# Kernel tuning notes

Measured on AMD Instinct MI355X. Metric: run time of the kernel, lower is better.

## Reference

```python
import jax, jax.numpy as jnp
from jax import lax
import numpy as np

T, B, I, H, O = 512, 128, 256, 512, 256


def setup_inputs() -> dict:
    key = jax.random.key(0)
    ks = jax.random.split(key, 11)
    s = 0.05
    return {
        "x": jax.random.normal(ks[0], (T, B, I), dtype=jnp.float32),
        "W_ih0": jax.random.normal(ks[1], (H, I), dtype=jnp.float32) * s,
        "b_ih0": jax.random.normal(ks[2], (H,), dtype=jnp.float32) * s,
        "W_hh0": jax.random.normal(ks[3], (H, H), dtype=jnp.float32) * s,
        "b_hh0": jax.random.normal(ks[4], (H,), dtype=jnp.float32) * s,
        "W_ih1": jax.random.normal(ks[5], (H, H), dtype=jnp.float32) * s,
        "b_ih1": jax.random.normal(ks[6], (H,), dtype=jnp.float32) * s,
        "W_hh1": jax.random.normal(ks[7], (H, H), dtype=jnp.float32) * s,
        "b_hh1": jax.random.normal(ks[8], (H,), dtype=jnp.float32) * s,
        "W_fc": jax.random.normal(ks[9], (O, H), dtype=jnp.float32) * s,
        "b_fc": jax.random.normal(ks[10], (O,), dtype=jnp.float32) * s,
    }


def reference(x, W_ih0, b_ih0, W_hh0, b_hh0, W_ih1, b_ih1, W_hh1, b_hh1, W_fc, b_fc):
    # x: [T, B, I] (batch_first=False). 2-layer tanh RNN via lax.scan over time.
    Tn, Bn, _ = x.shape
    Hn = W_hh0.shape[0]
    h0 = jnp.zeros((2, Bn, Hn), dtype=x.dtype)

    def step(h, xt):
        h1 = jnp.tanh(xt @ W_ih0.T + b_ih0 + h[0] @ W_hh0.T + b_hh0)  # [B, H]
        h2 = jnp.tanh(h1 @ W_ih1.T + b_ih1 + h[1] @ W_hh1.T + b_hh1)  # [B, H]
        return jnp.stack([h1, h2]), h2

    h_final, out = lax.scan(step, h0, x)  # out: [T, B, H]
    # Faithful to source: output[:, -1, :] indexes the LAST BATCH element (batch_first=False),
    # giving [T, H]; pred is [T, O].
    pred = out[:, -1, :] @ W_fc.T + b_fc
    return pred, h_final
```

## Files before the change

### kernel.cpp

```cpp
#include <hip/hip_runtime.h>
#include <hip/hip_bf16.h>

#define TT 512
#define BB 128
#define II 256
#define HH 512
#define OO 256

#define NGB 8
#define NGN 16
#define NS  32

#define PRED_SZ (TT*OO)

typedef __attribute__((ext_vector_type(8))) short bf16x8;
typedef __attribute__((ext_vector_type(4))) float f32x4;
typedef __attribute__((ext_vector_type(4))) int   i32x4;
typedef __attribute__((ext_vector_type(2))) int   i32x2;

#define WS_F1   0
#define WS_F2   1024
#define WS_H1   2048
#define WS_H2   (WS_H1 + 4*BB*HH*2)
#define WS_SAVE (WS_H2 + 2*BB*HH*2)
#define WS_ZERO WS_SAVE

__device__ __forceinline__ ushort f2bf(float f) {
  union { float f; unsigned u; } v; v.f = f;
  unsigned u = v.u;
  return (ushort)((u + 0x7FFFu + ((u >> 16) & 1u)) >> 16);
}

__device__ __forceinline__ float fast_tanh(float x) {
  float cx = fminf(fmaxf(x, -30.f), 30.f);
  float t  = __builtin_amdgcn_exp2f(cx * 2.885390081777927f);
  return (t - 1.f) * __builtin_amdgcn_rcpf(t + 1.f);
}

__device__ __forceinline__ i32x4 ld16(const ushort* p) {
  i32x4 r;
  asm volatile("global_load_dwordx4 %0, %1, off sc0 sc1" : "=v"(r) : "v"(p) : "memory");
  return r;
}
__device__ __forceinline__ f32x4 ld16g(const float* p) {
  f32x4 r;
  asm volatile("global_load_dwordx4 %0, %1, off" : "=v"(r) : "v"(p));
  return r;
}
__device__ __forceinline__ void st8(ushort* p, i32x2 v) {
  asm volatile("global_store_dwordx2 %0, %1, off sc0 sc1" :: "v"(p), "v"(v) : "memory");
}
__device__ __forceinline__ void st_flag(int* p, int v) {
  asm volatile("global_store_dword %0, %1, off sc0 sc1" :: "v"(p), "v"(v) : "memory");
}
__device__ __forceinline__ int ld_flag(const int* p) {
  int r;
  asm volatile("global_load_dword %0, %1, off sc0 sc1\n\ts_waitcnt vmcnt(0)"
               : "=v"(r) : "v"(p) : "memory");
  return r;
}
#define WAIT_VM(N) asm volatile("s_waitcnt vmcnt(" #N ")" ::: "memory")

__global__ __launch_bounds__(256, 1) void rnn_scan_kernel(
    const float* __restrict__ x,
    const float* __restrict__ Wih0, const float* __restrict__ bih0,
    const float* __restrict__ Whh0, const float* __restrict__ bhh0,
    const float* __restrict__ Wih1, const float* __restrict__ bih1,
    const float* __restrict__ Whh1, const float* __restrict__ bhh1,
    float* __restrict__ out, char* __restrict__ ws)
{
  __shared__ ushort ldsW[112*64*8];
  __shared__ float bias0[NS];
  __shared__ float bias1[NS];

  int*    flag1  = (int*)(ws + WS_F1);
  int*    flag2  = (int*)(ws + WS_F2);
  ushort* h1buf  = (ushort*)(ws + WS_H1);
  ushort* h2buf  = (ushort*)(ws + WS_H2);
  float*  h2save = (float*)(ws + WS_SAVE);

  const int tid  = threadIdx.x;
  const int bid  = blockIdx.x;
  const int gb   = bid & 7;
  const int gn   = bid >> 3;
  const int n0   = gn * NS;
  const int lane = tid & 63;

  {
    const int q = tid >> 6;
    #pragma unroll 1
    for (int u = 0; u < 112; ++u) {
      const float* Wsrc; int Km; int ul;
      if (u < 16)      { Wsrc = Wih0; Km = II; ul = u; }
      else if (u < 48) { Wsrc = Whh0; Km = HH; ul = u - 16; }
      else if (u < 80) { Wsrc = Wih1; Km = HH; ul = u - 48; }
      else             { Wsrc = Whh1; Km = HH; ul = u - 80; }
      const int nk  = Km >> 5;
      const int ttl = ul / nk;
      const int kk  = ul - ttl*nk;
      const int n   = n0 + ttl*16 + (lane & 15);
      const int k   = kk*32 + (lane >> 4)*8 + q*2;
      const float2 wv = *(const float2*)(Wsrc + (size_t)n*Km + k);
      ushort2 b2; b2.x = f2bf(wv.x); b2.y = f2bf(wv.y);
      *(ushort2*)&ldsW[(u*64 + lane)*8 + q*2] = b2;
    }
    if (tid < NS) {
      bias0[tid] = bih0[n0+tid] + bhh0[n0+tid];
      bias1[tid] = bih1[n0+tid] + bhh1[n0+tid];
    }
  }
  __syncthreads();

  const int w     = tid >> 6;
  const int ttile = w & 1;
  const int layer = w >> 1;
  const int kq    = lane >> 4;
  const int c     = lane & 15;
  const int rowg  = gb*16 + c;
  const int fl32  = lane & 31;
  const int nn    = ttile*16 + kq*4;
  int* f1g = flag1 + gb*32;
  int* f2g = flag2 + gb*32;
  const int myf = gn*2 + ttile;

  if (layer == 0) {
    f32x4 xacc = {0.f,0.f,0.f,0.f};
    {
      const float* xp = x + (size_t)rowg*II + kq*8;
      f32x4 xv[16];
      #pragma unroll
      for (int kk = 0; kk < 8; ++kk) {
        xv[2*kk]   = ld16g(xp + kk*32);
        xv[2*kk+1] = ld16g(xp + kk*32 + 4);
      }
      WAIT_VM(0);
      __builtin_amdgcn_sched_barrier(0);
      #pragma unroll
      for (int kk = 0; kk < 8; ++kk) {
        bf16x8 a;
        #pragma unroll
        for (int j = 0; j < 4; ++j) {
          a[j]   = (short)f2bf(xv[2*kk][j]);
          a[j+4] = (short)f2bf(xv[2*kk+1][j]);
        }
        const bf16x8 wf = *(const bf16x8*)&ldsW[((ttile*8 + kk)*64 + lane)*8];
        xacc = __builtin_amdgcn_mfma_f32_16x16x32_bf16(wf, a, xacc, 0, 0, 0);
      }
    }

    int vf1 = 0, vf2 = 0;
    for (int p = 0; p < TT; ++p) {
      if (p >= 1 && !__all(vf1 >= p)) {
        do { vf1 = ld_flag(f1g + fl32); } while (!__all(vf1 >= p));
      }
      if (p >= 4 && !__all(vf2 >= p-3)) {
        do { __builtin_amdgcn_s_sleep(1); vf2 = ld_flag(f2g + fl32); } while (!__all(vf2 >= p-3));
      }
      i32x4 af[16];
      if (p >= 1) {
        const ushort* ap = h1buf + ((size_t)((p-1)&3)*BB + rowg)*HH + kq*8;
        #pragma unroll
        for (int kk = 0; kk < 16; ++kk) af[kk] = ld16(ap + kk*32);
      }
      const int pn = (p+1 < TT) ? (p+1) : (TT-1);
      f32x4 xv[16];
      {
        const float* xp = x + ((size_t)pn*BB + rowg)*II + kq*8;
        #pragma unroll
        for (int kk = 0; kk < 8; ++kk) {
          xv[2*kk]   = ld16g(xp + kk*32);
          xv[2*kk+1] = ld16g(xp + kk*32 + 4);
        }
      }
      f32x4 ac1 = {0.f,0.f,0.f,0.f}, ac2 = {0.f,0.f,0.f,0.f};
      if (p >= 1) {
        WAIT_VM(16);
        __builtin_amdgcn_sched_barrier(0);
        #pragma unroll
        for (int kk = 0; kk < 8; ++kk) {
          const bf16x8 b0 = *(const bf16x8*)&ldsW[((16 + ttile*16 + kk)*64 + lane)*8];
          const bf16x8 b1 = *(const bf16x8*)&ldsW[((16 + ttile*16 + kk + 8)*64 + lane)*8];
          ac1 = __builtin_amdgcn_mfma_f32_16x16x32_bf16(b0, __builtin_bit_cast(bf16x8, af[kk]),   ac1, 0, 0, 0);
          ac2 = __builtin_amdgcn_mfma_f32_16x16x32_bf16(b1, __builtin_bit_cast(bf16x8, af[kk+8]), ac2, 0, 0, 0);
        }
      }
      float v0 = fast_tanh(xacc[0] + ac1[0] + ac2[0] + bias0[nn+0]);
      float v1 = fast_tanh(xacc[1] + ac1[1] + ac2[1] + bias0[nn+1]);
      float v2 = fast_tanh(xacc[2] + ac1[2] + ac2[2] + bias0[nn+2]);
      float v3 = fast_tanh(xacc[3] + ac1[3] + ac2[3] + bias0[nn+3]);
      i32x2 d;
      d[0] = (int)((unsigned)f2bf(v0) | ((unsigned)f2bf(v1) << 16));
      d[1] = (int)((unsigned)f2bf(v2) | ((unsigned)f2bf(v3) << 16));
      st8(h1buf + (size_t)(p&3)*BB*HH + (size_t)rowg*HH + n0 + nn, d);
      if (p == TT-1) {
        *(f32x4*)&out[PRED_SZ + (size_t)rowg*HH + n0 + nn] = (f32x4){v0,v1,v2,v3};
      }
      WAIT_VM(1);
      __builtin_amdgcn_sched_barrier(0);
      f32x4 xn = {0.f,0.f,0.f,0.f};
      #pragma unroll
      for (int kk = 0; kk < 8; ++kk) {
        bf16x8 a;
        #pragma unroll
        for (int j = 0; j < 4; ++j) {
          a[j]   = (short)f2bf(xv[2*kk][j]);
          a[j+4] = (short)f2bf(xv[2*kk+1][j]);
        }
        const bf16x8 wf = *(const bf16x8*)&ldsW[((ttile*8 + kk)*64 + lane)*8];
        xn = __builtin_amdgcn_mfma_f32_16x16x32_bf16(wf, a, xn, 0, 0, 0);
      }
      WAIT_VM(0);
      if (lane == 0) st_flag(&f1g[myf], p + 1);
      xacc = xn;
    }
  } else {
    int vf1 = 0, vf2 = 0;
    for (int p = 1; p <= TT; ++p) {
      if (!__all(vf1 >= p)) {
        do { vf1 = ld_flag(f1g + fl32); } while (!__all(vf1 >= p));
      }
      if (p >= 2 && !__all(vf2 >= p-1)) {
        do { vf2 = ld_flag(f2g + fl32); } while (!__all(vf2 >= p-1));
      }
      i32x4 af[16], a2[16];
      const ushort* ap  = h1buf + ((size_t)((p-1)&3)*BB + rowg)*HH + kq*8;
      const ushort* a2p = h2buf + ((size_t)(p&1)*BB + rowg)*HH + kq*8;
      #pragma unroll
      for (int kk = 0; kk < 16; ++kk) {
        af[kk] = ld16(ap  + kk*32);
        a2[kk] = ld16(a2p + kk*32);
      }
      WAIT_VM(0);
      __builtin_amdgcn_sched_barrier(0);

      f32x4 ac1 = {0.f,0.f,0.f,0.f}, ac2 = {0.f,0.f,0.f,0.f};
      f32x4 ac3 = {0.f,0.f,0.f,0.f}, ac4 = {0.f,0.f,0.f,0.f};
      #pragma unroll
      for (int kk = 0; kk < 8; ++kk) {
        const bf16x8 b0 = *(const bf16x8*)&ldsW[((48 + ttile*16 + kk)*64 + lane)*8];
        const bf16x8 b1 = *(const bf16x8*)&ldsW[((48 + ttile*16 + kk + 8)*64 + lane)*8];
        const bf16x8 b2 = *(const bf16x8*)&ldsW[((80 + ttile*16 + kk)*64 + lane)*8];
        const bf16x8 b3 = *(const bf16x8*)&ldsW[((80 + ttile*16 + kk + 8)*64 + lane)*8];
        ac1 = __builtin_amdgcn_mfma_f32_16x16x32_bf16(b0, __builtin_bit_cast(bf16x8, af[kk]),   ac1, 0, 0, 0);
        ac2 = __builtin_amdgcn_mfma_f32_16x16x32_bf16(b1, __builtin_bit_cast(bf16x8, af[kk+8]), ac2, 0, 0, 0);
        ac3 = __builtin_amdgcn_mfma_f32_16x16x32_bf16(b2, __builtin_bit_cast(bf16x8, a2[kk]),   ac3, 0, 0, 0);
        ac4 = __builtin_amdgcn_mfma_f32_16x16x32_bf16(b3, __builtin_bit_cast(bf16x8, a2[kk+8]), ac4, 0, 0, 0);
      }
      float v0 = fast_tanh(ac1[0] + ac2[0] + ac3[0] + ac4[0] + bias1[nn+0]);
      float v1 = fast_tanh(ac1[1] + ac2[1] + ac3[1] + ac4[1] + bias1[nn+1]);
      float v2 = fast_tanh(ac1[2] + ac2[2] + ac3[2] + ac4[2] + bias1[nn+2]);
      float v3 = fast_tanh(ac1[3] + ac2[3] + ac3[3] + ac4[3] + bias1[nn+3]);
      i32x2 d;
      d[0] = (int)((unsigned)f2bf(v0) | ((unsigned)f2bf(v1) << 16));
      d[1] = (int)((unsigned)f2bf(v2) | ((unsigned)f2bf(v3) << 16));
      st8(h2buf + (size_t)((p-1)&1)*BB*HH + (size_t)rowg*HH + n0 + nn, d);
      if (rowg == BB-1) {
        *(f32x4*)&h2save[(size_t)(p-1)*HH + n0 + nn] = (f32x4){v0,v1,v2,v3};
      }
      if (p == TT) {
        *(f32x4*)&out[PRED_SZ + BB*HH + (size_t)rowg*HH + n0 + nn] = (f32x4){v0,v1,v2,v3};
      }
      WAIT_VM(0);
      if (lane == 0) st_flag(&f2g[myf], p);
    }
  }
}

__global__ __launch_bounds__(256) void rnn_pred_kernel(
    const float* __restrict__ Wfc, const float* __restrict__ bfc,
    const float* __restrict__ h2save, float* __restrict__ out)
{
  __shared__ float hs[HH];
  const int t = blockIdx.x;
  for (int i = threadIdx.x; i < HH; i += 256) hs[i] = h2save[(size_t)t*HH + i];
  __syncthreads();
  const int o = threadIdx.x;
  const f32x4* wr = (const f32x4*)(Wfc + (size_t)o*HH);
  f32x4 s = {0.f,0.f,0.f,0.f};
  #pragma unroll 8
  for (int k = 0; k < HH/4; ++k) {
    const f32x4 wv = wr[k];
    const f32x4 hv = *(const f32x4*)&hs[4*k];
    s += wv * hv;
  }
  out[(size_t)t*OO + o] = bfc[o] + s[0] + s[1] + s[2] + s[3];
}

extern "C" void kernel_launch(void* const* d_in, const int* in_sizes, int n_in,
                              void* d_out, int out_size, void* d_ws, size_t ws_size,
                              hipStream_t stream) {
  const float* x    = (const float*)d_in[0];
  const float* Wih0 = (const float*)d_in[1];
  const float* bih0 = (const float*)d_in[2];
  const float* Whh0 = (const float*)d_in[3];
  const float* bhh0 = (const float*)d_in[4];
  const float* Wih1 = (const float*)d_in[5];
  const float* bih1 = (const float*)d_in[6];
  const float* Whh1 = (const float*)d_in[7];
  const float* bhh1 = (const float*)d_in[8];
  const float* Wfc  = (const float*)d_in[9];
  const float* bfc  = (const float*)d_in[10];
  float* out = (float*)d_out;
  char*  ws  = (char*)d_ws;

  hipMemsetAsync(ws, 0, WS_ZERO, stream);

  rnn_scan_kernel<<<NGB*NGN, 256, 0, stream>>>(x, Wih0, bih0, Whh0, bhh0,
                                               Wih1, bih1, Whh1, bhh1, out, ws);
  rnn_pred_kernel<<<TT, 256, 0, stream>>>(Wfc, bfc, (const float*)(ws + WS_SAVE), out);
}
```

Measured before the change: 3.912 ms.

## Replace per-step flag handshakes with tagged hidden-state words for inline validity

Each hidden-state element is stored as a 32-bit word holding the bf16 value in the high half and an 8-bit step tag in the low half. Consumers poll the data itself until every tag matches, which drops the separate layer-0 flag and the store-wait-flag round trip on the critical path. Layer-1 now signals consumption of h1 early, before its matmul, and the h2 ring buffer grows to four slots. In exchange the h1/h2 traffic doubles in size and byte-permute unpacking is added before each MFMA.

Result: slower. 5.513 ms (+40.9%).

```diff
diff --git a/kernel.cpp b/kernel.cpp
--- a/kernel.cpp
+++ b/kernel.cpp
@@ -16,14 +16,13 @@
 typedef __attribute__((ext_vector_type(8))) short bf16x8;
 typedef __attribute__((ext_vector_type(4))) float f32x4;
 typedef __attribute__((ext_vector_type(4))) int   i32x4;
-typedef __attribute__((ext_vector_type(2))) int   i32x2;
-
-#define WS_F1   0
-#define WS_F2   1024
+
+#define WS_F2   0
 #define WS_H1   2048
-#define WS_H2   (WS_H1 + 4*BB*HH*2)
-#define WS_SAVE (WS_H2 + 2*BB*HH*2)
+#define WS_H2   (WS_H1 + 4*BB*HH*4)
+#define WS_SAVE (WS_H2 + 4*BB*HH*4)
 #define WS_ZERO WS_SAVE
+
 
 __device__ __forceinline__ ushort f2bf(float f) {
   union { float f; unsigned u; } v; v.f = f;
@@ -37,7 +36,7 @@
   return (t - 1.f) * __builtin_amdgcn_rcpf(t + 1.f);
 }
 
-__device__ __forceinline__ i32x4 ld16(const ushort* p) {
+__device__ __forceinline__ i32x4 ld16f(const int* p) {
   i32x4 r;
   asm volatile("global_load_dwordx4 %0, %1, off sc0 sc1" : "=v"(r) : "v"(p) : "memory");
   return r;
@@ -47,8 +46,8 @@
   asm volatile("global_load_dwordx4 %0, %1, off" : "=v"(r) : "v"(p));
   return r;
 }
-__device__ __forceinline__ void st8(ushort* p, i32x2 v) {
-  asm volatile("global_store_dwordx2 %0, %1, off sc0 sc1" :: "v"(p), "v"(v) : "memory");
+__device__ __forceinline__ void st16(int* p, i32x4 v) {
+  asm volatile("global_store_dwordx4 %0, %1, off sc0 sc1" :: "v"(p), "v"(v) : "memory");
 }
 __device__ __forceinline__ void st_flag(int* p, int v) {
   asm volatile("global_store_dword %0, %1, off sc0 sc1" :: "v"(p), "v"(v) : "memory");
@@ -60,6 +59,16 @@
   return r;
 }
 #define WAIT_VM(N) asm volatile("s_waitcnt vmcnt(" #N ")" ::: "memory")
+
+__device__ __forceinline__ bf16x8 fragw(const i32x4* a, int q) {
+  const i32x4 lo = a[2*q], hi = a[2*q+1];
+  i32x4 r;
+  r[0] = (int)__builtin_amdgcn_perm((unsigned)lo[1], (unsigned)lo[0], 0x07060302u);
+  r[1] = (int)__builtin_amdgcn_perm((unsigned)lo[3], (unsigned)lo[2], 0x07060302u);
+  r[2] = (int)__builtin_amdgcn_perm((unsigned)hi[1], (unsigned)hi[0], 0x07060302u);
+  r[3] = (int)__builtin_amdgcn_perm((unsigned)hi[3], (unsigned)hi[2], 0x07060302u);
+  return __builtin_bit_cast(bf16x8, r);
+}
 
 __global__ __launch_bounds__(256, 1) void rnn_scan_kernel(
     const float* __restrict__ x,
@@ -73,11 +82,10 @@
   __shared__ float bias0[NS];
   __shared__ float bias1[NS];
 
-  int*    flag1  = (int*)(ws + WS_F1);
-  int*    flag2  = (int*)(ws + WS_F2);
-  ushort* h1buf  = (ushort*)(ws + WS_H1);
-  ushort* h2buf  = (ushort*)(ws + WS_H2);
-  float*  h2save = (float*)(ws + WS_SAVE);
+  int*   flag2  = (int*)(ws + WS_F2);
+  int*   h1f    = (int*)(ws + WS_H1);
+  int*   h2f    = (int*)(ws + WS_H2);
+  float* h2save = (float*)(ws + WS_SAVE);
 
   const int tid  = threadIdx.x;
   const int bid  = blockIdx.x;
@@ -119,7 +127,6 @@
   const int rowg  = gb*16 + c;
   const int fl32  = lane & 31;
   const int nn    = ttile*16 + kq*4;
-  int* f1g = flag1 + gb*32;
   int* f2g = flag2 + gb*32;
   const int myf = gn*2 + ttile;
 
@@ -148,19 +155,52 @@
       }
     }
 
-    int vf1 = 0, vf2 = 0;
+    int vf2 = 0;
     for (int p = 0; p < TT; ++p) {
-      if (p >= 1 && !__all(vf1 >= p)) {
-        do { vf1 = ld_flag(f1g + fl32); } while (!__all(vf1 >= p));
-      }
+      i32x4 af[32];
+      if (p >= 1) {
+        const int* ap = h1f + ((size_t)((p-1)&3)*BB + rowg)*HH + kq*8;
+        const int expl = p & 255;
+        const int* f2p = f2g + fl32;
+        for (;;) {
+          #pragma unroll
+          for (int kk = 0; kk < 16; ++kk) {
+            af[2*kk]   = ld16f(ap + kk*32);
+            af[2*kk+1] = ld16f(ap + kk*32 + 4);
+          }
+          int f2v = vf2;
+          if (p >= 4) {
+            asm volatile("global_load_dword %0, %1, off sc0 sc1" : "=v"(f2v) : "v"(f2p) : "memory");
+          }
+          WAIT_VM(0);
+          __builtin_amdgcn_sched_barrier(0);
+          int bad = 0;
+          #pragma unroll
+          for (int q = 0; q < 32; ++q)
+            bad |= (af[q][0]^expl) | (af[q][1]^expl) | (af[q][2]^expl) | (af[q][3]^expl);
+          vf2 = f2v;
+          if (__all((bad & 255) == 0)) break;
+          __builtin_amdgcn_s_sleep(1);
+        }
+      }
+      f32x4 ac1 = {0.f,0.f,0.f,0.f}, ac2 = {0.f,0.f,0.f,0.f};
+      if (p >= 1) {
+        #pragma unroll
+        for (int kk = 0; kk < 8; ++kk) {
+          const bf16x8 a0 = fragw(af, kk);
+          const bf16x8 a1 = fragw(af, kk+8);
+          const bf16x8 b0 = *(const bf16x8*)&ldsW[((16 + ttile*16 + kk)*64 + lane)*8];
+          const bf16x8 b1 = *(const bf16x8*)&ldsW[((16 + ttile*16 + kk + 8)*64 + lane)*8];
+          ac1 = __builtin_amdgcn_mfma_f32_16x16x32_bf16(b0, a0, ac1, 0, 0, 0);
+          ac2 = __builtin_amdgcn_mfma_f32_16x16x32_bf16(b1, a1, ac2, 0, 0, 0);
+        }
+      }
+      const float v0 = fast_tanh(xacc[0] + ac1[0] + ac2[0] + bias0[nn+0]);
+      const float v1 = fast_tanh(xacc[1] + ac1[1] + ac2[1] + bias0[nn+1]);
+      const float v2 = fast_tanh(xacc[2] + ac1[2] + ac2[2] + bias0[nn+2]);
+      const float v3 = fast_tanh(xacc[3] + ac1[3] + ac2[3] + bias0[nn+3]);
       if (p >= 4 && !__all(vf2 >= p-3)) {
-        do { __builtin_amdgcn_s_sleep(1); vf2 = ld_flag(f2g + fl32); } while (!__all(vf2 >= p-3));
-      }
-      i32x4 af[16];
-      if (p >= 1) {
-        const ushort* ap = h1buf + ((size_t)((p-1)&3)*BB + rowg)*HH + kq*8;
-        #pragma unroll
-        for (int kk = 0; kk < 16; ++kk) af[kk] = ld16(ap + kk*32);
+        do { vf2 = ld_flag(f2g + fl32); } while (!__all(vf2 >= p-3));
       }
       const int pn = (p+1 < TT) ? (p+1) : (TT-1);
       f32x4 xv[16];
@@ -172,29 +212,13 @@
           xv[2*kk+1] = ld16g(xp + kk*32 + 4);
         }
       }
-      f32x4 ac1 = {0.f,0.f,0.f,0.f}, ac2 = {0.f,0.f,0.f,0.f};
-      if (p >= 1) {
-        WAIT_VM(16);
-        __builtin_amdgcn_sched_barrier(0);
-        #pragma unroll
-        for (int kk = 0; kk < 8; ++kk) {
-          const bf16x8 b0 = *(const bf16x8*)&ldsW[((16 + ttile*16 + kk)*64 + lane)*8];
-          const bf16x8 b1 = *(const bf16x8*)&ldsW[((16 + ttile*16 + kk + 8)*64 + lane)*8];
-          ac1 = __builtin_amdgcn_mfma_f32_16x16x32_bf16(b0, __builtin_bit_cast(bf16x8, af[kk]),   ac1, 0, 0, 0);
-          ac2 = __builtin_amdgcn_mfma_f32_16x16x32_bf16(b1, __builtin_bit_cast(bf16x8, af[kk+8]), ac2, 0, 0, 0);
-        }
-      }
-      float v0 = fast_tanh(xacc[0] + ac1[0] + ac2[0] + bias0[nn+0]);
-      float v1 = fast_tanh(xacc[1] + ac1[1] + ac2[1] + bias0[nn+1]);
-      float v2 = fast_tanh(xacc[2] + ac1[2] + ac2[2] + bias0[nn+2]);
-      float v3 = fast_tanh(xacc[3] + ac1[3] + ac2[3] + bias0[nn+3]);
-      i32x2 d;
-      d[0] = (int)((unsigned)f2bf(v0) | ((unsigned)f2bf(v1) << 16));
-      d[1] = (int)((unsigned)f2bf(v2) | ((unsigned)f2bf(v3) << 16));
-      st8(h1buf + (size_t)(p&3)*BB*HH + (size_t)rowg*HH + n0 + nn, d);
-      if (p == TT-1) {
-        *(f32x4*)&out[PRED_SZ + (size_t)rowg*HH + n0 + nn] = (f32x4){v0,v1,v2,v3};
-      }
+      const int tg = (p+1) & 255;
+      i32x4 d;
+      d[0] = ((int)(unsigned)f2bf(v0) << 16) | tg;
+      d[1] = ((int)(unsigned)f2bf(v1) << 16) | tg;
+      d[2] = ((int)(unsigned)f2bf(v2) << 16) | tg;
+      d[3] = ((int)(unsigned)f2bf(v3) << 16) | tg;
+      st16(h1f + (size_t)(p&3)*BB*HH + (size_t)rowg*HH + n0 + nn, d);
       WAIT_VM(1);
       __builtin_amdgcn_sched_barrier(0);
       f32x4 xn = {0.f,0.f,0.f,0.f};
@@ -209,59 +233,90 @@
         const bf16x8 wf = *(const bf16x8*)&ldsW[((ttile*8 + kk)*64 + lane)*8];
         xn = __builtin_amdgcn_mfma_f32_16x16x32_bf16(wf, a, xn, 0, 0, 0);
       }
-      WAIT_VM(0);
-      if (lane == 0) st_flag(&f1g[myf], p + 1);
       xacc = xn;
+      if (p == TT-1) {
+        *(f32x4*)&out[PRED_SZ + (size_t)rowg*HH + n0 + nn] = (f32x4){v0,v1,v2,v3};
+      }
     }
   } else {
-    int vf1 = 0, vf2 = 0;
     for (int p = 1; p <= TT; ++p) {
-      if (!__all(vf1 >= p)) {
-        do { vf1 = ld_flag(f1g + fl32); } while (!__all(vf1 >= p));
-      }
-      if (p >= 2 && !__all(vf2 >= p-1)) {
-        do { vf2 = ld_flag(f2g + fl32); } while (!__all(vf2 >= p-1));
-      }
-      i32x4 af[16], a2[16];
-      const ushort* ap  = h1buf + ((size_t)((p-1)&3)*BB + rowg)*HH + kq*8;
-      const ushort* a2p = h2buf + ((size_t)(p&1)*BB + rowg)*HH + kq*8;
-      #pragma unroll
-      for (int kk = 0; kk < 16; ++kk) {
-        af[kk] = ld16(ap  + kk*32);
-        a2[kk] = ld16(a2p + kk*32);
-      }
-      WAIT_VM(0);
-      __builtin_amdgcn_sched_barrier(0);
+      bf16x8 fa2[16];
+      {
+        i32x4 a2[32];
+        const int* a2p = h2f + ((size_t)((p+2)&3)*BB + rowg)*HH + kq*8;
+        const int expl = (p-1) & 255;
+        for (;;) {
+          #pragma unroll
+          for (int kk = 0; kk < 16; ++kk) {
+            a2[2*kk]   = ld16f(a2p + kk*32);
+            a2[2*kk+1] = ld16f(a2p + kk*32 + 4);
+          }
+          WAIT_VM(0);
+          __builtin_amdgcn_sched_barrier(0);
+          int bad = 0;
+          #pragma unroll
+          for (int q = 0; q < 32; ++q)
+            bad |= (a2[q][0]^expl) | (a2[q][1]^expl) | (a2[q][2]^expl) | (a2[q][3]^expl);
+          if (__all((bad & 255) == 0)) break;
+          __builtin_amdgcn_s_sleep(1);
+        }
+        #pragma unroll
+        for (int kk = 0; kk < 16; ++kk) fa2[kk] = fragw(a2, kk);
+      }
+      i32x4 af[32];
+      {
+        const int* ap = h1f + ((size_t)((p-1)&3)*BB + rowg)*HH + kq*8;
+        const int expl = p & 255;
+        for (;;) {
+          #pragma unroll
+          for (int kk = 0; kk < 16; ++kk) {
+            af[2*kk]   = ld16f(ap + kk*32);
+            af[2*kk+1] = ld16f(ap + kk*32 + 4);
+          }
+          WAIT_VM(0);
+          __builtin_amdgcn_sched_barrier(0);
+          int bad = 0;
+          #pragma unroll
+          for (int q = 0; q < 32; ++q)
+            bad |= (af[q][0]^expl) | (af[q][1]^expl) | (af[q][2]^expl) | (af[q][3]^expl);
+          if (__all((bad & 255) == 0)) break;
+          __builtin_amdgcn_s_sleep(1);
+        }
+      }
+      if (lane == 0) st_flag(&f2g[myf], p);
 
       f32x4 ac1 = {0.f,0.f,0.f,0.f}, ac2 = {0.f,0.f,0.f,0.f};
       f32x4 ac3 = {0.f,0.f,0.f,0.f}, ac4 = {0.f,0.f,0.f,0.f};
       #pragma unroll
       for (int kk = 0; kk < 8; ++kk) {
+        const bf16x8 a0 = fragw(af, kk);
+        const bf16x8 a1 = fragw(af, kk+8);
         const bf16x8 b0 = *(const bf16x8*)&ldsW[((48 + ttile*16 + kk)*64 + lane)*8];
         const bf16x8 b1 = *(const bf16x8*)&ldsW[((48 + ttile*16 + kk + 8)*64 + lane)*8];
         const bf16x8 b2 = *(const bf16x8*)&ldsW[((80 + ttile*16 + kk)*64 + lane)*8];
         const bf16x8 b3 = *(const bf16x8*)&ldsW[((80 + ttile*16 + kk + 8)*64 + lane)*8];
-        ac1 = __builtin_amdgcn_mfma_f32_16x16x32_bf16(b0, __builtin_bit_cast(bf16x8, af[kk]),   ac1, 0, 0, 0);
-        ac2 = __builtin_amdgcn_mfma_f32_16x16x32_bf16(b1, __builtin_bit_cast(bf16x8, af[kk+8]), ac2, 0, 0, 0);
-        ac3 = __builtin_amdgcn_mfma_f32_16x16x32_bf16(b2, __builtin_bit_cast(bf16x8, a2[kk]),   ac3, 0, 0, 0);
-        ac4 = __builtin_amdgcn_mfma_f32_16x16x32_bf16(b3, __builtin_bit_cast(bf16x8, a2[kk+8]), ac4, 0, 0, 0);
-      }
-      float v0 = fast_tanh(ac1[0] + ac2[0] + ac3[0] + ac4[0] + bias1[nn+0]);
-      float v1 = fast_tanh(ac1[1] + ac2[1] + ac3[1] + ac4[1] + bias1[nn+1]);
-      float v2 = fast_tanh(ac1[2] + ac2[2] + ac3[2] + ac4[2] + bias1[nn+2]);
-      float v3 = fast_tanh(ac1[3] + ac2[3] + ac3[3] + ac4[3] + bias1[nn+3]);
-      i32x2 d;
-      d[0] = (int)((unsigned)f2bf(v0) | ((unsigned)f2bf(v1) << 16));
-      d[1] = (int)((unsigned)f2bf(v2) | ((unsigned)f2bf(v3) << 16));
-      st8(h2buf + (size_t)((p-1)&1)*BB*HH + (size_t)rowg*HH + n0 + nn, d);
+        ac1 = __builtin_amdgcn_mfma_f32_16x16x32_bf16(b0, a0, ac1, 0, 0, 0);
+        ac2 = __builtin_amdgcn_mfma_f32_16x16x32_bf16(b1, a1, ac2, 0, 0, 0);
+        ac3 = __builtin_amdgcn_mfma_f32_16x16x32_bf16(b2, fa2[kk],   ac3, 0, 0, 0);
+        ac4 = __builtin_amdgcn_mfma_f32_16x16x32_bf16(b3, fa2[kk+8], ac4, 0, 0, 0);
+      }
+      const float v0 = fast_tanh(ac1[0] + ac2[0] + ac3[0] + ac4[0] + bias1[nn+0]);
+      const float v1 = fast_tanh(ac1[1] + ac2[1] + ac3[1] + ac4[1] + bias1[nn+1]);
+      const float v2 = fast_tanh(ac1[2] + ac2[2] + ac3[2] + ac4[2] + bias1[nn+2]);
+      const float v3 = fast_tanh(ac1[3] + ac2[3] + ac3[3] + ac4[3] + bias1[nn+3]);
+      const int tg = p & 255;
+      i32x4 d;
+      d[0] = ((int)(unsigned)f2bf(v0) << 16) | tg;
+      d[1] = ((int)(unsigned)f2bf(v1) << 16) | tg;
+      d[2] = ((int)(unsigned)f2bf(v2) << 16) | tg;
+      d[3] = ((int)(unsigned)f2bf(v3) << 16) | tg;
+      st16(h2f + (size_t)((p-1)&3)*BB*HH + (size_t)rowg*HH + n0 + nn, d);
       if (rowg == BB-1) {
         *(f32x4*)&h2save[(size_t)(p-1)*HH + n0 + nn] = (f32x4){v0,v1,v2,v3};
       }
       if (p == TT) {
         *(f32x4*)&out[PRED_SZ + BB*HH + (size_t)rowg*HH + n0 + nn] = (f32x4){v0,v1,v2,v3};
       }
-      WAIT_VM(0);
-      if (lane == 0) st_flag(&f2g[myf], p);
     }
   }
 }
```
